# Kernel optimization log

Hardware: AMD Instinct MI355X
Metric: run time of the kernel (lower is better)

Reference implementation:

```python
import jax, jax.numpy as jnp
import numpy as np

N_SAT = 1536
N_UAV = 1536
D = 64


def setup_inputs() -> dict:
    key = jax.random.key(0)
    ks = jax.random.split(key, 8)
    sat_regions = jax.random.normal(ks[0], (N_SAT, D), dtype=jnp.float32)
    uav_regions = jax.random.normal(ks[1], (N_UAV, D), dtype=jnp.float32)
    # weights in [in, out] layout (transpose of torch Linear), scaled like kaiming-ish init
    W1 = jax.random.normal(ks[2], (2 * D, D), dtype=jnp.float32) / np.sqrt(2 * D)
    b1 = jnp.zeros((D,), dtype=jnp.float32)
    W2 = jax.random.normal(ks[3], (D, D // 2), dtype=jnp.float32) / np.sqrt(D)
    b2 = jnp.zeros((D // 2,), dtype=jnp.float32)
    W3 = jax.random.normal(ks[4], (D // 2, 1), dtype=jnp.float32) / np.sqrt(D // 2)
    b3 = jnp.zeros((1,), dtype=jnp.float32)
    return {"sat_regions": sat_regions, "uav_regions": uav_regions,
            "W1": W1, "b1": b1, "W2": W2, "b2": b2, "W3": W3, "b3": b3}


def reference(sat_regions, uav_regions, W1, b1, W2, b2, W3, b3):
    d = sat_regions.shape[-1]
    # Layer 1 on concat([sat, uav]) == sat @ W1[:d] + uav @ W1[d:], broadcast over pairs.
    h_sat = sat_regions @ W1[:d]            # [N, D]
    h_uav = uav_regions @ W1[d:]            # [M, D]
    h1 = jax.nn.relu(h_sat[:, None, :] + h_uav[None, :, :] + b1)   # [N, M, D]
    h2 = jax.nn.relu(h1 @ W2 + b2)                                  # [N, M, D/2]
    sim = jax.nn.sigmoid((h2 @ W3 + b3)[..., 0])                    # [N, M]

    # Greedy bipartite assignment: for each sat row in order, pick best unused uav.
    def step(mask, row):
        scores = jnp.where(mask, row, jnp.float32(-1.0))  # used entries set to -1, as in torch
        j = jnp.argmax(scores)
        return mask.at[j].set(False), j

    mask0 = jnp.ones((sim.shape[1],), dtype=bool)
    _, assign = jax.lax.scan(step, mask0, sim)            # assign: [N] int32
    matched_uav = uav_regions[assign]                      # [N, D]
    # aligned_pairs as a stacked array: [N, 2, D] = (sat_i, uav_{assign[i]})
    return jnp.stack([sat_regions, matched_uav], axis=1)
```

## Files before the change

### kernel.cpp

```cpp
#include <hip/hip_runtime.h>
#include <float.h>

#define NS 1536
#define DD 64

static const size_t OFF_A  = 0;
static const size_t OFF_C2 = 98304;
static const size_t OFF_L  = 196608;
static const size_t OFF_AS = 196608 + (size_t)NS * NS;

__global__ __launch_bounds__(64) void kA(const float* __restrict__ sat,
                                         const float* __restrict__ uav,
                                         const float* __restrict__ W1,
                                         const float* __restrict__ b1,
                                         float* __restrict__ A,
                                         float* __restrict__ C2) {
    const int row = blockIdx.x;
    const int d = threadIdx.x;
    float accA = b1[d];
    float accC = 0.f;
    const float* __restrict__ satr = sat + row * DD;
    const float* __restrict__ uavr = uav + row * DD;
#pragma unroll 8
    for (int k = 0; k < DD; ++k) {
        accA = fmaf(satr[k], W1[k * DD + d], accA);
        accC = fmaf(uavr[k], W1[(DD + k) * DD + d], accC);
    }
    A[row * DD + d] = accA;
    C2[((size_t)(d >> 2) * NS + row) * 4 + (d & 3)] = accC;
}

__global__ __launch_bounds__(256) void kB(const float* __restrict__ A,
                                          const float* __restrict__ C2,
                                          const float* __restrict__ W2,
                                          const float* __restrict__ b2,
                                          const float* __restrict__ W3,
                                          float* __restrict__ L) {
    const int lane = threadIdx.x & 63;
    const int wave = threadIdx.x >> 6;
    const int i = __builtin_amdgcn_readfirstlane(blockIdx.x * 4 + wave);
    const int jbase = blockIdx.y * 256;
    const float* __restrict__ Ar = A + (size_t)i * DD;

    float u[4][32];
#pragma unroll
    for (int o = 0; o < 32; ++o) {
        const float b = b2[o];
        u[0][o] = b; u[1][o] = b; u[2][o] = b; u[3][o] = b;
    }

    const float4* __restrict__ C2v = (const float4*)C2;

    for (int d4 = 0; d4 < 16; ++d4) {
        float c[4][4];
#pragma unroll
        for (int p = 0; p < 4; ++p) {
            const float4 t = C2v[(size_t)d4 * NS + jbase + p * 64 + lane];
            c[p][0] = t.x; c[p][1] = t.y; c[p][2] = t.z; c[p][3] = t.w;
        }
#pragma unroll
        for (int dd = 0; dd < 4; ++dd) {
            const float a = Ar[d4 * 4 + dd];
            const float v0 = fmaxf(a + c[0][dd], 0.f);
            const float v1 = fmaxf(a + c[1][dd], 0.f);
            const float v2 = fmaxf(a + c[2][dd], 0.f);
            const float v3 = fmaxf(a + c[3][dd], 0.f);
            const float* __restrict__ w2r = W2 + (d4 * 4 + dd) * 32;
#pragma unroll
            for (int o = 0; o < 32; ++o) {
                const float w = w2r[o];
                u[0][o] = fmaf(v0, w, u[0][o]);
                u[1][o] = fmaf(v1, w, u[1][o]);
                u[2][o] = fmaf(v2, w, u[2][o]);
                u[3][o] = fmaf(v3, w, u[3][o]);
            }
        }
    }

#pragma unroll
    for (int p = 0; p < 4; ++p) {
        float acc = 0.f;
#pragma unroll
        for (int o = 0; o < 32; ++o)
            acc = fmaf(fmaxf(u[p][o], 0.f), W3[o], acc);
        L[(size_t)i * NS + jbase + p * 64 + lane] = acc;
    }
}

__global__ __launch_bounds__(256) void kC(const float* __restrict__ L,
                                          unsigned short* __restrict__ top) {
    __shared__ int hist[256];
    __shared__ int suff[256];
    __shared__ float cv[1024];
    __shared__ int ci[1024];
    __shared__ int s_cnt, s_B0, s_base, s_B1;
    const int t = threadIdx.x;
    const int row = blockIdx.x;
    const float* __restrict__ Lr = L + (size_t)row * NS;

    top[row * 256 + t] = 0xFFFFu;

    hist[t] = 0;
    if (t == 0) s_cnt = 0;
    __syncthreads();

    unsigned ub[6]; float fv[6];
#pragma unroll
    for (int k = 0; k < 6; ++k) {
        const float x = Lr[t + 256 * k];
        fv[k] = x;
        unsigned b = __float_as_uint(x);
        b = (b & 0x80000000u) ? ~b : (b | 0x80000000u);
        ub[k] = b;
        atomicAdd(&hist[b >> 24], 1);
    }
    __syncthreads();

    suff[t] = hist[t];
    __syncthreads();
    for (int off = 1; off < 256; off <<= 1) {
        const int v = (t + off < 256) ? suff[t + off] : 0;
        __syncthreads();
        suff[t] += v;
        __syncthreads();
    }
    if (suff[t] >= 256 && (t == 255 || suff[t + 1] < 256)) {
        s_B0 = t;
        s_base = (t == 255) ? 0 : suff[t + 1];
    }
    __syncthreads();
    const unsigned B0 = (unsigned)s_B0;
    const int base = s_base;

    hist[t] = 0;
    __syncthreads();
#pragma unroll
    for (int k = 0; k < 6; ++k)
        if ((ub[k] >> 24) == B0) atomicAdd(&hist[(ub[k] >> 16) & 255], 1);
    __syncthreads();
    suff[t] = hist[t];
    __syncthreads();
    for (int off = 1; off < 256; off <<= 1) {
        const int v = (t + off < 256) ? suff[t + off] : 0;
        __syncthreads();
        suff[t] += v;
        __syncthreads();
    }
    const int need = 256 - base;
    if (suff[t] >= need && (t == 255 || suff[t + 1] < need)) s_B1 = t;
    __syncthreads();
    const unsigned B1 = (unsigned)s_B1;
    const int m = base + suff[B1];
    if (m > 1024) return;

#pragma unroll
    for (int k = 0; k < 6; ++k) {
        const unsigned hi = ub[k] >> 24;
        const unsigned mid = (ub[k] >> 16) & 255u;
        if (hi > B0 || (hi == B0 && mid >= B1)) {
            const int pos = atomicAdd(&s_cnt, 1);
            cv[pos] = fv[k];
            ci[pos] = t + 256 * k;
        }
    }
    __syncthreads();

    for (int e = t; e < m; e += 256) {
        const float v = cv[e]; const int id = ci[e];
        int r = 0;
        for (int s2 = 0; s2 < m; ++s2) {
            const float vs = cv[s2];
            if (vs > v || (vs == v && ci[s2] < id)) ++r;
        }
        if (r < 256) top[row * 256 + (r & 63) * 4 + (r >> 6)] = (unsigned short)id;
    }
}

__device__ __forceinline__ unsigned wave_max_u32_dpp(unsigned x) {
    unsigned t;
    t = (unsigned)__builtin_amdgcn_update_dpp(0, (int)x, 0x111, 0xF, 0xF, true);
    x = x > t ? x : t;
    t = (unsigned)__builtin_amdgcn_update_dpp(0, (int)x, 0x112, 0xF, 0xF, true);
    x = x > t ? x : t;
    t = (unsigned)__builtin_amdgcn_update_dpp(0, (int)x, 0x114, 0xF, 0xF, true);
    x = x > t ? x : t;
    t = (unsigned)__builtin_amdgcn_update_dpp(0, (int)x, 0x118, 0xF, 0xF, true);
    x = x > t ? x : t;
    t = (unsigned)__builtin_amdgcn_update_dpp(0, (int)x, 0x142, 0xF, 0xF, true);
    x = x > t ? x : t;
    t = (unsigned)__builtin_amdgcn_update_dpp(0, (int)x, 0x143, 0xF, 0xF, true);
    x = x > t ? x : t;
    return x;
}

__device__ __forceinline__ int fb_argmax(const float* __restrict__ L, int i,
                                         int mU, const int (&U8)[8],
                                         const int* used_s,
                                         const unsigned short* U_s, int lane) {
    const float* __restrict__ Lr = L + (size_t)i * NS;
    float bv = -FLT_MAX; int bi = NS;
    {
        int idx[8]; int flc[8]; float vv[8];
#pragma unroll
        for (int c = 0; c < 8; ++c) {
            const int k = lane + (c << 6);
            idx[c] = (k < mU) ? U8[c] : 0;
        }
#pragma unroll
        for (int c = 0; c < 8; ++c) vv[c] = Lr[idx[c]];
#pragma unroll
        for (int c = 0; c < 8; ++c) flc[c] = used_s[idx[c]];
#pragma unroll
        for (int c = 0; c < 8; ++c) {
            const int k = lane + (c << 6);
            if (k < mU && flc[c] == 0 &&
                (vv[c] > bv || (vv[c] == bv && idx[c] < bi))) {
                bv = vv[c]; bi = idx[c];
            }
        }
    }
    for (int kbase = 512; kbase < mU; kbase += 512) {
        int idx[8]; int flc[8]; float vv[8];
#pragma unroll
        for (int c = 0; c < 8; ++c) {
            const int k = kbase + lane + (c << 6);
            idx[c] = (k < mU) ? (int)U_s[k] : 0;
        }
#pragma unroll
        for (int c = 0; c < 8; ++c) flc[c] = used_s[idx[c]];
#pragma unroll
        for (int c = 0; c < 8; ++c) vv[c] = Lr[idx[c]];
#pragma unroll
        for (int c = 0; c < 8; ++c) {
            const int k = kbase + lane + (c << 6);
            if (k < mU && flc[c] == 0 &&
                (vv[c] > bv || (vv[c] == bv && idx[c] < bi))) {
                bv = vv[c]; bi = idx[c];
            }
        }
    }
    unsigned b = __float_as_uint(bv);
    unsigned key = (b & 0x80000000u) ? ~b : (b | 0x80000000u);
    const unsigned wk = wave_max_u32_dpp(key);
    const unsigned maxk = (unsigned)__builtin_amdgcn_readlane((int)wk, 63);
    unsigned cand = (key == maxk) ? (unsigned)(NS - bi) : 0u;
    const unsigned wc = wave_max_u32_dpp(cand);
    const unsigned mc = (unsigned)__builtin_amdgcn_readlane((int)wc, 63);
    return NS - (int)mc;
}

__global__ __launch_bounds__(64) void kD(const float* __restrict__ L,
                                         const unsigned short* __restrict__ top,
                                         int* __restrict__ assign) {
    __shared__ int used_s[NS];
    __shared__ int assign_s[NS];
    __shared__ unsigned short U_s[NS];
    const int lane = threadIdx.x;
    for (int k = lane; k < NS; k += 64) used_s[k] = 0;
    __syncthreads();

    const uint2* __restrict__ T = (const uint2*)top;

    uint2 buf[16];
#pragma unroll
    for (int k = 0; k < 16; ++k) buf[k] = T[k * 64 + lane];

    int f0 = 0, f1 = 0, f2 = 0, f3 = 0;
    int jprev = -1;
    int mU = NS;
    int U8[8];
    bool tight = false;

    for (int g = 0; g < NS; g += 8) {
        if ((g & 63) == 0) {
            int fl[24];
#pragma unroll
            for (int k = 0; k < 24; ++k) fl[k] = used_s[lane + (k << 6)];
            int cnt = 0;
#pragma unroll
            for (int k = 0; k < 24; ++k) cnt += (fl[k] == 0);
            int incl = cnt;
#pragma unroll
            for (int o = 1; o < 64; o <<= 1) {
                const int v = __shfl_up(incl, o);
                if (lane >= o) incl += v;
            }
            int pos = incl - cnt;
#pragma unroll
            for (int k = 0; k < 24; ++k) {
                if (fl[k] == 0) { U_s[pos] = (unsigned short)(lane + (k << 6)); ++pos; }
            }
            mU = __builtin_amdgcn_readlane(incl, 63);
#pragma unroll
            for (int c = 0; c < 8; ++c) U8[c] = (int)U_s[lane + (c << 6)];
        }

        if (!tight) {
            uint2 nb[8];
#pragma unroll
            for (int k = 0; k < 8; ++k) {
                int r = g + 16 + k;
                r = (r < NS) ? r : (NS - 1);
                nb[k] = T[r * 64 + lane];
            }

            int fbcnt = 0;
#pragma unroll
            for (int q = 0; q < 8; ++q) {
                const int i = g + q;

                const uint2 pn = buf[q + 1];
                const int n0 = (int)(pn.x & 0xFFFFu), n1 = (int)(pn.x >> 16);
                const int n2 = (int)(pn.y & 0xFFFFu), n3 = (int)(pn.y >> 16);
                const int g0 = used_s[n0 < NS ? n0 : 0];
                const int g1 = used_s[n1 < NS ? n1 : 0];
                const int g2 = used_s[n2 < NS ? n2 : 0];
                const int g3 = used_s[n3 < NS ? n3 : 0];

                const uint2 pc = buf[q];
                const int c0 = (int)(pc.x & 0xFFFFu), c1 = (int)(pc.x >> 16);
                const int c2 = (int)(pc.y & 0xFFFFu), c3 = (int)(pc.y >> 16);
                const bool a0 = (c0 < NS) && (f0 == 0) && (c0 != jprev);
                const bool a1 = (c1 < NS) && (f1 == 0) && (c1 != jprev);
                const bool a2 = (c2 < NS) && (f2 == 0) && (c2 != jprev);
                const bool a3 = (c3 < NS) && (f3 == 0) && (c3 != jprev);
                const unsigned long long b0 = __ballot(a0);
                const unsigned long long b1 = __ballot(a1);
                const unsigned long long b2 = __ballot(a2);
                const unsigned long long b3 = __ballot(a3);

                int j;
                if (b0)      j = __builtin_amdgcn_readlane(c0, __ffsll(b0) - 1);
                else if (b1) j = __builtin_amdgcn_readlane(c1, __ffsll(b1) - 1);
                else if (b2) j = __builtin_amdgcn_readlane(c2, __ffsll(b2) - 1);
                else if (b3) j = __builtin_amdgcn_readlane(c3, __ffsll(b3) - 1);
                else {
                    ++fbcnt;
                    j = fb_argmax(L, i, mU, U8, used_s, U_s, lane);
                }
                if (lane == 0) { used_s[j] = 1; assign_s[i] = j; }
                jprev = j;
                f0 = g0; f1 = g1; f2 = g2; f3 = g3;
            }

#pragma unroll
            for (int k = 0; k < 8; ++k) buf[k] = buf[k + 8];
#pragma unroll
            for (int k = 0; k < 8; ++k) buf[k + 8] = nb[k];

            tight = (fbcnt == 8);
        } else {
#pragma unroll 1
            for (int q = 0; q < 8; ++q) {
                const int i = g + q;
                const int j = fb_argmax(L, i, mU, U8, used_s, U_s, lane);
                if (lane == 0) { used_s[j] = 1; assign_s[i] = j; }
            }
        }
    }

    for (int k = lane; k < NS; k += 64) assign[k] = assign_s[k];
}

__global__ __launch_bounds__(128) void kE(const float* __restrict__ sat,
                                          const float* __restrict__ uav,
                                          const int* __restrict__ assign,
                                          float* __restrict__ out) {
    const int i = blockIdx.x;
    const int t = threadIdx.x;
    if (t < 64) out[(size_t)i * 128 + t] = sat[(size_t)i * DD + t];
    else        out[(size_t)i * 128 + t] = uav[(size_t)assign[i] * DD + (t - 64)];
}

extern "C" void kernel_launch(void* const* d_in, const int* in_sizes, int n_in,
                              void* d_out, int out_size, void* d_ws, size_t ws_size,
                              hipStream_t stream) {
    const float* sat = (const float*)d_in[0];
    const float* uav = (const float*)d_in[1];
    const float* W1  = (const float*)d_in[2];
    const float* b1  = (const float*)d_in[3];
    const float* W2  = (const float*)d_in[4];
    const float* b2  = (const float*)d_in[5];
    const float* W3  = (const float*)d_in[6];

    float* ws = (float*)d_ws;
    float* A   = ws + OFF_A;
    float* C2  = ws + OFF_C2;
    float* L   = ws + OFF_L;
    int* assign = (int*)(ws + OFF_AS);
    unsigned short* top = (unsigned short*)(ws + OFF_A);

    hipLaunchKernelGGL(kA, dim3(NS), dim3(64), 0, stream, sat, uav, W1, b1, A, C2);
    hipLaunchKernelGGL(kB, dim3(NS / 4, NS / 256), dim3(256), 0, stream,
                       A, C2, W2, b2, W3, L);
    hipLaunchKernelGGL(kC, dim3(NS), dim3(256), 0, stream, L, top);
    hipLaunchKernelGGL(kD, dim3(1), dim3(64), 0, stream, L, top, assign);
    hipLaunchKernelGGL(kE, dim3(NS), dim3(128), 0, stream, sat, uav, assign,
                       (float*)d_out);
}
```

Before: 808.3 us.

## Prefetch gathered score rows four steps ahead in tight greedy phase

```diff
diff --git a/kernel.cpp b/kernel.cpp
--- a/kernel.cpp
+++ b/kernel.cpp
@@ -193,52 +193,7 @@
     return x;
 }
 
-__device__ __forceinline__ int fb_argmax(const float* __restrict__ L, int i,
-                                         int mU, const int (&U8)[8],
-                                         const int* used_s,
-                                         const unsigned short* U_s, int lane) {
-    const float* __restrict__ Lr = L + (size_t)i * NS;
-    float bv = -FLT_MAX; int bi = NS;
-    {
-        int idx[8]; int flc[8]; float vv[8];
-#pragma unroll
-        for (int c = 0; c < 8; ++c) {
-            const int k = lane + (c << 6);
-            idx[c] = (k < mU) ? U8[c] : 0;
-        }
-#pragma unroll
-        for (int c = 0; c < 8; ++c) vv[c] = Lr[idx[c]];
-#pragma unroll
-        for (int c = 0; c < 8; ++c) flc[c] = used_s[idx[c]];
-#pragma unroll
-        for (int c = 0; c < 8; ++c) {
-            const int k = lane + (c << 6);
-            if (k < mU && flc[c] == 0 &&
-                (vv[c] > bv || (vv[c] == bv && idx[c] < bi))) {
-                bv = vv[c]; bi = idx[c];
-            }
-        }
-    }
-    for (int kbase = 512; kbase < mU; kbase += 512) {
-        int idx[8]; int flc[8]; float vv[8];
-#pragma unroll
-        for (int c = 0; c < 8; ++c) {
-            const int k = kbase + lane + (c << 6);
-            idx[c] = (k < mU) ? (int)U_s[k] : 0;
-        }
-#pragma unroll
-        for (int c = 0; c < 8; ++c) flc[c] = used_s[idx[c]];
-#pragma unroll
-        for (int c = 0; c < 8; ++c) vv[c] = Lr[idx[c]];
-#pragma unroll
-        for (int c = 0; c < 8; ++c) {
-            const int k = kbase + lane + (c << 6);
-            if (k < mU && flc[c] == 0 &&
-                (vv[c] > bv || (vv[c] == bv && idx[c] < bi))) {
-                bv = vv[c]; bi = idx[c];
-            }
-        }
-    }
+__device__ __forceinline__ int dpp_argmax(float bv, int bi) {
     unsigned b = __float_as_uint(bv);
     unsigned key = (b & 0x80000000u) ? ~b : (b | 0x80000000u);
     const unsigned wk = wave_max_u32_dpp(key);
@@ -249,6 +204,73 @@
     return NS - (int)mc;
 }
 
+__device__ __forceinline__ int fb_argmax(const float* __restrict__ L, int i,
+                                         int mU, const int (&U16)[16],
+                                         const int* used_s,
+                                         const unsigned short* U_s, int lane) {
+    const float* __restrict__ Lr = L + (size_t)i * NS;
+    float bv = -FLT_MAX; int bi = NS;
+    {
+        int idx[8]; int flc[8]; float vv[8];
+#pragma unroll
+        for (int c = 0; c < 8; ++c) {
+            const int k = lane + (c << 6);
+            idx[c] = (k < mU) ? U16[c] : 0;
+        }
+#pragma unroll
+        for (int c = 0; c < 8; ++c) vv[c] = Lr[idx[c]];
+#pragma unroll
+        for (int c = 0; c < 8; ++c) flc[c] = used_s[idx[c]];
+#pragma unroll
+        for (int c = 0; c < 8; ++c) {
+            const int k = lane + (c << 6);
+            if (k < mU && flc[c] == 0 &&
+                (vv[c] > bv || (vv[c] == bv && idx[c] < bi))) {
+                bv = vv[c]; bi = idx[c];
+            }
+        }
+    }
+    for (int kbase = 512; kbase < mU; kbase += 512) {
+        int idx[8]; int flc[8]; float vv[8];
+#pragma unroll
+        for (int c = 0; c < 8; ++c) {
+            const int k = kbase + lane + (c << 6);
+            idx[c] = (k < mU) ? (int)U_s[k] : 0;
+        }
+#pragma unroll
+        for (int c = 0; c < 8; ++c) flc[c] = used_s[idx[c]];
+#pragma unroll
+        for (int c = 0; c < 8; ++c) vv[c] = Lr[idx[c]];
+#pragma unroll
+        for (int c = 0; c < 8; ++c) {
+            const int k = kbase + lane + (c << 6);
+            if (k < mU && flc[c] == 0 &&
+                (vv[c] > bv || (vv[c] == bv && idx[c] < bi))) {
+                bv = vv[c]; bi = idx[c];
+            }
+        }
+    }
+    return dpp_argmax(bv, bi);
+}
+
+__device__ __forceinline__ int tight_consume(const float (&pv)[16],
+                                             const int (&U16)[16], int mU,
+                                             const int* used_s, int lane) {
+    int fl[16];
+#pragma unroll
+    for (int c = 0; c < 16; ++c) fl[c] = used_s[U16[c]];
+    float bv = -FLT_MAX; int bi = NS;
+#pragma unroll
+    for (int c = 0; c < 16; ++c) {
+        const int k = lane + (c << 6);
+        if (k < mU && fl[c] == 0 &&
+            (pv[c] > bv || (pv[c] == bv && U16[c] < bi))) {
+            bv = pv[c]; bi = U16[c];
+        }
+    }
+    return dpp_argmax(bv, bi);
+}
+
 __global__ __launch_bounds__(64) void kD(const float* __restrict__ L,
                                          const unsigned short* __restrict__ top,
                                          int* __restrict__ assign) {
@@ -268,8 +290,11 @@
     int f0 = 0, f1 = 0, f2 = 0, f3 = 0;
     int jprev = -1;
     int mU = NS;
-    int U8[8];
+    int U16[16];
     bool tight = false;
+    bool cover = false;
+    float pv0[16], pv1[16], pv2[16], pv3[16];
+    int pvalid0 = 0, pvalid1 = 0, pvalid2 = 0, pvalid3 = 0;
 
     for (int g = 0; g < NS; g += 8) {
         if ((g & 63) == 0) {
@@ -292,7 +317,9 @@
             }
             mU = __builtin_amdgcn_readlane(incl, 63);
 #pragma unroll
-            for (int c = 0; c < 8; ++c) U8[c] = (int)U_s[lane + (c << 6)];
+            for (int c = 0; c < 16; ++c) U16[c] = (int)U_s[lane + (c << 6)];
+            cover = (mU <= 1024);
+            pvalid0 = pvalid1 = pvalid2 = pvalid3 = 0;
         }
 
         if (!tight) {
@@ -336,7 +363,7 @@
                 else if (b3) j = __builtin_amdgcn_readlane(c3, __ffsll(b3) - 1);
                 else {
                     ++fbcnt;
-                    j = fb_argmax(L, i, mU, U8, used_s, U_s, lane);
+                    j = fb_argmax(L, i, mU, U16, used_s, U_s, lane);
                 }
                 if (lane == 0) { used_s[j] = 1; assign_s[i] = j; }
                 jprev = j;
@@ -350,12 +377,30 @@
 
             tight = (fbcnt == 8);
         } else {
-#pragma unroll 1
-            for (int q = 0; q < 8; ++q) {
-                const int i = g + q;
-                const int j = fb_argmax(L, i, mU, U8, used_s, U_s, lane);
-                if (lane == 0) { used_s[j] = 1; assign_s[i] = j; }
-            }
+#define TROW(Q, PV, PVALID)                                                   \
+            {                                                                 \
+                const int i = g + (Q);                                        \
+                int j;                                                        \
+                if (PVALID) j = tight_consume(PV, U16, mU, used_s, lane);     \
+                else        j = fb_argmax(L, i, mU, U16, used_s, U_s, lane);  \
+                if (lane == 0) { used_s[j] = 1; assign_s[i] = j; }            \
+                if (cover && (i + 4) < NS) {                                  \
+                    const float* __restrict__ Lr2 = L + (size_t)(i + 4) * NS; \
+                    _Pragma("unroll")                                         \
+                    for (int c = 0; c < 16; ++c) PV[c] = Lr2[U16[c]];         \
+                    PVALID = 1;                                               \
+                } else PVALID = 0;                                            \
+                __builtin_amdgcn_sched_barrier(0);                            \
+            }
+            TROW(0, pv0, pvalid0)
+            TROW(1, pv1, pvalid1)
+            TROW(2, pv2, pvalid2)
+            TROW(3, pv3, pvalid3)
+            TROW(4, pv0, pvalid0)
+            TROW(5, pv1, pvalid1)
+            TROW(6, pv2, pvalid2)
+            TROW(7, pv3, pvalid3)
+#undef TROW
         }
     }
 
```

Result: slower. 869.1 us (+7.5%).
